# Optimization experiments

Hardware: AMD Instinct MI355X
Metric: run time of the kernel (lower is better)

Reference implementation:

```python
import jax, jax.numpy as jnp
import numpy as np

B, S, D = 2, 2048, 1024
H, DH = 16, 64
DM = 4096
NEG = 1e10


def setup_inputs() -> dict:
    key = jax.random.key(0)
    ks = jax.random.split(key, 8)
    sc = 1.0 / np.sqrt(D)
    return {
        "x": jax.random.normal(ks[0], (B, S, D), jnp.float32),
        "W_Q": jax.random.normal(ks[1], (H, DH, D), jnp.float32) * sc,
        "W_K": jax.random.normal(ks[2], (H, DH, D), jnp.float32) * sc,
        "W_V": jax.random.normal(ks[3], (H, DH, D), jnp.float32) * sc,
        "W_O": jax.random.normal(ks[4], (D, H * DH), jnp.float32) * sc,
        "W_in": jax.random.normal(ks[5], (DM, D), jnp.float32) * sc,
        "b_in": jnp.zeros((DM,), jnp.float32),
        "W_out": jax.random.normal(ks[6], (D, DM), jnp.float32) * sc,
        "b_out": jnp.zeros((D,), jnp.float32),
    }


def reference(x, W_Q, W_K, W_V, W_O, W_in, b_in, W_out, b_out):
    b, s, d = x.shape
    d_head = W_Q.shape[1]
    # --- Attention (faithful to original einsum/mask formulation) ---
    q = jnp.einsum('ihd,bpd->biph', W_Q, x)
    k = jnp.einsum('ihd,bpd->biph', W_K, x)
    v = jnp.einsum('ihd,bpd->biph', W_V, x)
    scores = jnp.einsum('biph,biqh->biqp', k, q)  # [b,i,q,p]
    # original: t.tril(scores) - 1e10 * (1 - triu(ones)) ; mask buffer is triu
    triu = jnp.triu(jnp.ones((s, s), x.dtype))
    masked = jnp.tril(scores) - NEG * (1.0 - triu)
    attn = jax.nn.softmax(masked / np.sqrt(d_head), axis=-1)
    z = jnp.einsum('biph,biqp->biqh', v, attn)          # [b,i,q,h]
    z_flat = z.transpose(0, 2, 1, 3).reshape(b, s, -1)   # b q (i h)
    attn_out = jnp.einsum('df,bqf->bqd', W_O, z_flat)
    # --- Block residual structure (as written: x = attn(x); x = x + x) ---
    mid = attn_out + attn_out
    # --- MLP ---
    pre = jnp.einsum('md,bpd->bpm', W_in, mid) + b_in
    h = jax.nn.relu(pre)
    mlp_out = jnp.einsum('dm,bpm->bpd', W_out, h) + b_out
    return mid + mlp_out
```

## Files before the change

### kernel.cpp

```cpp
#include <hip/hip_runtime.h>
#include <hip/hip_bf16.h>
#include <stdint.h>

typedef unsigned short ushort_t;
typedef __attribute__((ext_vector_type(8))) short short8;
typedef __attribute__((ext_vector_type(4))) float floatx4;

#define DEV __device__ __forceinline__

DEV ushort_t f2b(float f) {
  uint32_t x = __float_as_uint(f);
  uint32_t r = (x + 0x7FFFu + ((x >> 16) & 1u)) >> 16;
  return (ushort_t)r;
}
DEV float b2f(ushort_t u) { return __uint_as_float(((uint32_t)u) << 16); }

DEV void async16(const ushort_t* g, ushort_t* l) {
  __builtin_amdgcn_global_load_lds(
      (const __attribute__((address_space(1))) void*)g,
      (__attribute__((address_space(3))) void*)l, 16, 0, 0);
}

struct Cvt7 {
  const float* src[7];
  ushort_t* dst[7];
  float scale[7];
  unsigned start[8];
};
__global__ void cvt_all(Cvt7 a) {
  unsigned idx = blockIdx.x * blockDim.x + threadIdx.x;
  if (idx >= a.start[7]) return;
  int seg = 0;
#pragma unroll
  for (int j = 1; j < 7; j++) seg += (idx >= a.start[j]) ? 1 : 0;
  unsigned off = idx - a.start[seg];
  float sc = a.scale[seg];
  float4 v = ((const float4*)a.src[seg])[off];
  ((ushort4*)a.dst[seg])[off] =
      make_ushort4(f2b(v.x * sc), f2b(v.y * sc), f2b(v.z * sc), f2b(v.w * sc));
}

template <int MODE, int MT, int SWZ>
__launch_bounds__(256)
__global__ void gemm_bt(const ushort_t* __restrict__ A, const ushort_t* __restrict__ Bm,
                        int M, int N, int Kd, int ldk,
                        ushort_t* __restrict__ outB, float* __restrict__ outF,
                        const float* __restrict__ bias) {
  constexpr int TM = 32 * MT;
  __shared__ alignas(16) ushort_t As[TM * 64];
  __shared__ alignas(16) ushort_t Bs[128 * 64];
  const int tid = threadIdx.x;
  const int wave = tid >> 6, lane = tid & 63;
  const int wm = wave >> 1, wn = wave & 1;

  int bx, by;
  if constexpr (SWZ == 1) {
    const int f = blockIdx.x + gridDim.x * blockIdx.y;
    by = (f & 7) + 8 * (f / (8 * gridDim.x));
    bx = (f >> 3) % gridDim.x;
  } else if constexpr (SWZ == 2) {
    const int x = blockIdx.x, y = blockIdx.y;
    bx = 2 * (x & 3) + (y & 1);
    by = (y >> 1) + 32 * (x >> 2);
  } else {
    bx = blockIdx.x; by = blockIdx.y;
  }
  const int m0 = by * TM, n0 = bx * 128;
  const int kz = blockIdx.z * Kd;

  floatx4 acc[MT][4];
#pragma unroll
  for (int i = 0; i < MT; i++)
#pragma unroll
    for (int j = 0; j < 4; j++) acc[i][j] = (floatx4){0.f, 0.f, 0.f, 0.f};

  const int r8 = lane >> 3;
  const int scol = (((lane & 7) ^ (r8 & 7)) * 8);
  const ushort_t* gA = A + (size_t)(m0 + wave * (TM / 4) + r8) * ldk + kz + scol;
  const ushort_t* gB = Bm + (size_t)(n0 + wave * 32 + r8) * ldk + kz + scol;
  ushort_t* lA = As + wave * (TM / 4) * 64;
  ushort_t* lB = Bs + wave * 2048;

  const int fr = lane & 15, fq = lane >> 4;
  const int sw = fr & 7;
  const ushort_t* rdA = As + (wm * 16 * MT + fr) * 64;
  const ushort_t* rdB = Bs + (wn * 64 + fr) * 64;

  for (int k0 = 0; k0 < Kd; k0 += 64) {
#pragma unroll
    for (int j = 0; j < MT; j++) async16(gA + (size_t)j * 8 * ldk, lA + j * 512);
#pragma unroll
    for (int j = 0; j < 4; j++) async16(gB + (size_t)j * 8 * ldk, lB + j * 512);
    gA += 64; gB += 64;
    __syncthreads();
#pragma unroll
    for (int h = 0; h < 2; h++) {
      const int co = ((h * 4 + fq) ^ sw) * 8;
      short8 af[MT], bfv[4];
#pragma unroll
      for (int mt = 0; mt < MT; mt++) af[mt] = *(const short8*)(rdA + mt * 16 * 64 + co);
#pragma unroll
      for (int nt = 0; nt < 4; nt++) bfv[nt] = *(const short8*)(rdB + nt * 16 * 64 + co);
#pragma unroll
      for (int mt = 0; mt < MT; mt++)
#pragma unroll
        for (int nt = 0; nt < 4; nt++)
          acc[mt][nt] = __builtin_amdgcn_mfma_f32_16x16x32_bf16(af[mt], bfv[nt], acc[mt][nt], 0, 0, 0);
    }
    __syncthreads();
  }

  const int crow = m0 + wm * 16 * MT + (lane >> 4) * 4;
  const int ccol = n0 + wn * 64 + (lane & 15);
  const size_t zoff = (size_t)blockIdx.z * M * N;
#pragma unroll
  for (int mt = 0; mt < MT; mt++)
#pragma unroll
    for (int nt = 0; nt < 4; nt++) {
      floatx4 a = acc[mt][nt];
#pragma unroll
      for (int r = 0; r < 4; r++) {
        const int gm = crow + mt * 16 + r;
        const int gn = ccol + nt * 16;
        const size_t idx = (size_t)gm * N + gn;
        float v = a[r];
        if constexpr (MODE == 0) {
          outB[idx] = f2b(v);
        } else if constexpr (MODE == 1) {
          outB[idx] = f2b(v);
          outF[idx] = v + bias[gn];
        } else if constexpr (MODE == 2) {
          float t = v + bias[gn];
          outB[idx] = f2b(t > 0.f ? t : 0.f);
        } else {
          outF[zoff + idx] = v;
        }
      }
    }
}

__launch_bounds__(256)
__global__ void reduce2(const float4* __restrict__ P, float4* __restrict__ out, int n4) {
  int i = blockIdx.x * blockDim.x + threadIdx.x;
  int st = gridDim.x * blockDim.x;
  for (; i < n4; i += st) {
    float4 a = out[i];
    float4 p0 = P[i], p1 = P[i + 1048576];
    a.x += p0.x + p1.x;
    a.y += p0.y + p1.y;
    a.z += p0.z + p1.z;
    a.w += p0.w + p1.w;
    out[i] = a;
  }
}

__launch_bounds__(256)
__global__ void attn1(const ushort_t* __restrict__ qkv,
                      float* __restrict__ eG, float* __restrict__ psumG) {
  const int c = blockIdx.x & 63;
  const int i = (blockIdx.x >> 6) & 15;
  const int b = blockIdx.x >> 10;
  const int t = threadIdx.x, wave = t >> 6, h = t & 63;
  const size_t rowbase = (size_t)b * 2048 * 3072;
  float vacc = 0.f;
#pragma unroll
  for (int r = 0; r < 8; r++) {
    const int s = c * 32 + wave * 8 + r;
    const size_t rb = rowbase + (size_t)s * 3072 + i * 64 + h;
    float q = b2f(qkv[rb]);
    float k = b2f(qkv[rb + 1024]);
    float v = b2f(qkv[rb + 2048]);
    float d = q * k;
#pragma unroll
    for (int off = 32; off > 0; off >>= 1) d += __shfl_xor(d, off, 64);
    if (h == 0) eG[((size_t)(b * 16 + i)) * 2048 + s] = __expf(d * 0.125f);
    vacc += v;
  }
  __shared__ float vs[4][64];
  vs[wave][h] = vacc;
  __syncthreads();
  if (t < 64)
    psumG[(((size_t)(b * 16 + i)) * 64 + c) * 64 + t] =
        vs[0][t] + vs[1][t] + vs[2][t] + vs[3][t];
}

__launch_bounds__(256)
__global__ void attn2(const ushort_t* __restrict__ qkv,
                      const float* __restrict__ eG, const float* __restrict__ psumG,
                      ushort_t* __restrict__ Z) {
  const int wave = threadIdx.x >> 6, h = threadIdx.x & 63;
  const int c = (blockIdx.x & 15) * 4 + wave;
  const int i = (blockIdx.x >> 4) & 15;
  const int b = blockIdx.x >> 8;
  const size_t rowbase = (size_t)b * 2048 * 3072;
  const size_t pbase = ((size_t)(b * 16 + i)) * 64;
  float run = 0.f;
#pragma unroll 8
  for (int cc = c + 1; cc < 64; cc++) run += psumG[(pbase + cc) * 64 + h];
  const size_t ebase = ((size_t)(b * 16 + i)) * 2048;
  for (int t4 = 1; t4 >= 0; t4--) {
    float vv[16], ee[16];
#pragma unroll
    for (int j = 0; j < 16; j++) {
      const int s = c * 32 + t4 * 16 + j;
      vv[j] = b2f(qkv[rowbase + (size_t)s * 3072 + 2048 + i * 64 + h]);
      ee[j] = eG[ebase + s];
    }
#pragma unroll
    for (int j = 15; j >= 0; j--) {
      const int s = c * 32 + t4 * 16 + j;
      float z = (ee[j] * vv[j] + run) / (ee[j] + (float)(2047 - s));
      Z[((size_t)b * 2048 + s) * 1024 + i * 64 + h] = f2b(z);
      run += vv[j];
    }
  }
}

extern "C" void kernel_launch(void* const* d_in, const int* in_sizes, int n_in,
                              void* d_out, int out_size, void* d_ws, size_t ws_size,
                              hipStream_t stream) {
  const float* x     = (const float*)d_in[0];
  const float* W_Q   = (const float*)d_in[1];
  const float* W_K   = (const float*)d_in[2];
  const float* W_V   = (const float*)d_in[3];
  const float* W_O   = (const float*)d_in[4];
  const float* W_in  = (const float*)d_in[5];
  const float* b_in  = (const float*)d_in[6];
  const float* W_out = (const float*)d_in[7];
  const float* b_out = (const float*)d_in[8];
  float* out = (float*)d_out;

  char* base = (char*)d_ws;
  const size_t MB = 1048576;
  ushort_t* Xb    = (ushort_t*)(base + 0 * MB);
  ushort_t* Wqkv  = (ushort_t*)(base + 8 * MB);
  ushort_t* WOb   = (ushort_t*)(base + 14 * MB);
  ushort_t* Z     = (ushort_t*)(base + 16 * MB);
  ushort_t* QKV   = (ushort_t*)(base + 24 * MB);
  ushort_t* midb  = (ushort_t*)(base + 48 * MB);
  ushort_t* Winb  = (ushort_t*)(base + 56 * MB);
  ushort_t* Woutb = (ushort_t*)(base + 64 * MB);
  ushort_t* Hb    = (ushort_t*)(base + 72 * MB);
  float*    P     = (float*)(base + 0 * MB);
  float*    psumG = (float*)(base + 72 * MB);
  float*    eG    = (float*)(base + 72 * MB + 524288);

  Cvt7 ca;
  ca.src[0] = x;     ca.dst[0] = Xb;               ca.scale[0] = 1.f;
  ca.src[1] = W_Q;   ca.dst[1] = Wqkv;             ca.scale[1] = 1.f;
  ca.src[2] = W_K;   ca.dst[2] = Wqkv + 1048576;   ca.scale[2] = 1.f;
  ca.src[3] = W_V;   ca.dst[3] = Wqkv + 2097152;   ca.scale[3] = 1.f;
  ca.src[4] = W_O;   ca.dst[4] = WOb;              ca.scale[4] = 2.f;
  ca.src[5] = W_in;  ca.dst[5] = Winb;             ca.scale[5] = 1.f;
  ca.src[6] = W_out; ca.dst[6] = Woutb;            ca.scale[6] = 1.f;
  unsigned n4s[7] = {1048576, 262144, 262144, 262144, 262144, 1048576, 1048576};
  unsigned acc4 = 0;
  for (int j = 0; j < 7; j++) { ca.start[j] = acc4; acc4 += n4s[j]; }
  ca.start[7] = acc4;
  cvt_all<<<dim3((acc4 + 255) / 256), dim3(256), 0, stream>>>(ca);

  gemm_bt<0, 4, 0><<<dim3(24, 32), 256, 0, stream>>>(Xb, Wqkv, 4096, 3072, 1024, 1024,
                                                     QKV, nullptr, nullptr);
  attn1<<<dim3(2048), 256, 0, stream>>>(QKV, eG, psumG);
  attn2<<<dim3(512), 256, 0, stream>>>(QKV, eG, psumG, Z);
  gemm_bt<1, 2, 1><<<dim3(8, 64), 256, 0, stream>>>(Z, WOb, 4096, 1024, 1024, 1024,
                                                    midb, out, b_out);
  gemm_bt<2, 4, 0><<<dim3(32, 32), 256, 0, stream>>>(midb, Winb, 4096, 4096, 1024, 1024,
                                                     Hb, nullptr, b_in);
  gemm_bt<3, 2, 2><<<dim3(8, 64, 2), 256, 0, stream>>>(Hb, Woutb, 4096, 1024, 2048, 4096,
                                                       nullptr, P, nullptr);
  reduce2<<<dim3(1024), 256, 0, stream>>>((const float4*)P, (float4*)out, 1048576);
}
```

Measured before the change: 289.6 us.

## Add 256x256-tile 512-thread GEMM with 4-stage async LDS pipeline for QKV and MLP

Introduces a new GEMM kernel with 256x256 output tiles, 8 waves, a 4-deep global-to-LDS async buffer ring, a swizzled LDS layout and XCD-aware block remapping. It replaces the QKV, MLP-in and MLP-out GEMMs. The MLP-out GEMM moves from split-K by 2 to split-K by 4, and the final reduction is widened to match. Larger tiles raise data reuse per load, but with only 192 or 256 blocks the grid may underfill the CUs. The split-K by 4 path also adds partial-sum traffic through the extra reduction.

```diff
diff --git a/kernel.cpp b/kernel.cpp
--- a/kernel.cpp
+++ b/kernel.cpp
@@ -139,17 +139,149 @@
     }
 }
 
+template <int MODE>
+__launch_bounds__(512, 2)
+__global__ void gemm256(const ushort_t* __restrict__ A, const ushort_t* __restrict__ Bm,
+                        int M, int N, int Kd, int ldk,
+                        ushort_t* __restrict__ outB, float* __restrict__ outF,
+                        const float* __restrict__ bias) {
+  __shared__ alignas(16) ushort_t As[4][256 * 32];
+  __shared__ alignas(16) ushort_t Bs[4][256 * 32];
+  const int tid = threadIdx.x;
+  const int lane = tid & 63;
+  const int wave = tid >> 6;
+  const int wm = wave >> 2, wn = wave & 3;
+
+  const int gy = gridDim.y;
+  int f = blockIdx.x + gridDim.x * blockIdx.y;
+  {
+    const int nwg = gridDim.x * gy;
+    const int q = nwg >> 3, rr = nwg & 7;
+    const int xcd = f & 7, ix = f >> 3;
+    f = (xcd < rr ? xcd * (q + 1) : rr * (q + 1) + (xcd - rr) * q) + ix;
+  }
+  const int bx = f / gy, by = f - gy * bx;
+  const int m0 = by * 256, n0 = bx * 256;
+  const size_t kz = (size_t)blockIdx.z * Kd;
+
+  floatx4 acc[8][4];
+#pragma unroll
+  for (int i = 0; i < 8; i++)
+#pragma unroll
+    for (int j = 0; j < 4; j++) acc[i][j] = (floatx4){0.f, 0.f, 0.f, 0.f};
+
+  const int rloc = tid >> 2, cch = tid & 3;
+  const int gcol = ((cch ^ ((rloc >> 1) & 3)) * 8);
+  const ushort_t* gA = A + (size_t)(m0 + rloc) * ldk + kz + gcol;
+  const ushort_t* gB = Bm + (size_t)(n0 + rloc) * ldk + kz + gcol;
+  const int lofs = rloc * 32 + cch * 8;
+
+#define STGA32(bufi, kofs)                                              \
+  {                                                                     \
+    async16(gA + (kofs), &As[bufi][lofs]);                              \
+    async16(gA + (size_t)128 * ldk + (kofs), &As[bufi][4096 + lofs]);   \
+  }
+#define STGB32(bufi, kofs)                                              \
+  {                                                                     \
+    async16(gB + (kofs), &Bs[bufi][lofs]);                              \
+    async16(gB + (size_t)128 * ldk + (kofs), &Bs[bufi][4096 + lofs]);   \
+  }
+
+  const int NT = Kd >> 5;
+  STGA32(0, 0) STGB32(0, 0)
+  if (NT > 1) { STGA32(1, 32) STGB32(1, 32) }
+  if (NT > 2) { STGA32(2, 64) STGB32(2, 64) }
+  if (NT > 2) asm volatile("s_waitcnt vmcnt(8)" ::: "memory");
+  else if (NT > 1) asm volatile("s_waitcnt vmcnt(4)" ::: "memory");
+  else asm volatile("s_waitcnt vmcnt(0)" ::: "memory");
+  __builtin_amdgcn_s_barrier();
+
+  const int fr = lane & 15, fq = lane >> 4;
+  const int co = ((fq ^ ((fr >> 1) & 3)) * 8);
+  const int aoff = (wm * 128 + fr) * 32 + co;
+  const int boff = (wn * 64 + fr) * 32 + co;
+
+  for (int kt = 0; kt < NT; ++kt) {
+    const int cb = kt & 3;
+    const int pb = (kt + 3) & 3;
+    const int kof = (kt + 3) * 32;
+    const bool sp = (kt + 3) < NT;
+    const ushort_t* Ab = As[cb];
+    const ushort_t* Bb = Bs[cb];
+    short8 av[4], bv[4];
+
+#pragma unroll
+    for (int i = 0; i < 4; i++) av[i] = *(const short8*)(Ab + aoff + i * 512);
+#pragma unroll
+    for (int j = 0; j < 4; j++) bv[j] = *(const short8*)(Bb + boff + j * 512);
+    if (sp) STGA32(pb, kof)
+    __builtin_amdgcn_s_barrier();
+    asm volatile("s_waitcnt lgkmcnt(0)" ::: "memory");
+    __builtin_amdgcn_s_setprio(1);
+#pragma unroll
+    for (int i = 0; i < 4; i++)
+#pragma unroll
+      for (int j = 0; j < 4; j++)
+        acc[i][j] = __builtin_amdgcn_mfma_f32_16x16x32_bf16(av[i], bv[j], acc[i][j], 0, 0, 0);
+    __builtin_amdgcn_s_setprio(0);
+    __builtin_amdgcn_s_barrier();
+
+#pragma unroll
+    for (int i = 0; i < 4; i++) av[i] = *(const short8*)(Ab + aoff + 2048 + i * 512);
+    if (sp) STGB32(pb, kof)
+    __builtin_amdgcn_s_barrier();
+    asm volatile("s_waitcnt lgkmcnt(0)" ::: "memory");
+    __builtin_amdgcn_s_setprio(1);
+#pragma unroll
+    for (int i = 0; i < 4; i++)
+#pragma unroll
+      for (int j = 0; j < 4; j++)
+        acc[4 + i][j] = __builtin_amdgcn_mfma_f32_16x16x32_bf16(av[i], bv[j], acc[4 + i][j], 0, 0, 0);
+    __builtin_amdgcn_s_setprio(0);
+    if (kt + 3 < NT) asm volatile("s_waitcnt vmcnt(8)" ::: "memory");
+    else if (kt + 2 < NT) asm volatile("s_waitcnt vmcnt(4)" ::: "memory");
+    else asm volatile("s_waitcnt vmcnt(0)" ::: "memory");
+    __builtin_amdgcn_s_barrier();
+  }
+#undef STGA32
+#undef STGB32
+
+  const int crow = m0 + wm * 128 + (lane >> 4) * 4;
+  const int ccol = n0 + wn * 64 + (lane & 15);
+  const size_t zoff = (size_t)blockIdx.z * ((size_t)M * (size_t)N);
+#pragma unroll
+  for (int mt = 0; mt < 8; mt++)
+#pragma unroll
+    for (int nt = 0; nt < 4; nt++) {
+      floatx4 a = acc[mt][nt];
+#pragma unroll
+      for (int r = 0; r < 4; r++) {
+        const int gm = crow + mt * 16 + r;
+        const int gn = ccol + nt * 16;
+        const size_t idx = (size_t)gm * N + gn;
+        if constexpr (MODE == 0) {
+          outB[idx] = f2b(a[r]);
+        } else if constexpr (MODE == 2) {
+          float t = a[r] + bias[gn];
+          outB[idx] = f2b(t > 0.f ? t : 0.f);
+        } else {
+          outF[zoff + idx] = a[r];
+        }
+      }
+    }
+}
+
 __launch_bounds__(256)
-__global__ void reduce2(const float4* __restrict__ P, float4* __restrict__ out, int n4) {
+__global__ void reduce4(const float4* __restrict__ P, float4* __restrict__ out, int n4) {
   int i = blockIdx.x * blockDim.x + threadIdx.x;
   int st = gridDim.x * blockDim.x;
   for (; i < n4; i += st) {
     float4 a = out[i];
-    float4 p0 = P[i], p1 = P[i + 1048576];
-    a.x += p0.x + p1.x;
-    a.y += p0.y + p1.y;
-    a.z += p0.z + p1.z;
-    a.w += p0.w + p1.w;
+    float4 p0 = P[i], p1 = P[i + 1048576], p2 = P[i + 2097152], p3 = P[i + 3145728];
+    a.x += (p0.x + p1.x) + (p2.x + p3.x);
+    a.y += (p0.y + p1.y) + (p2.y + p3.y);
+    a.z += (p0.z + p1.z) + (p2.z + p3.z);
+    a.w += (p0.w + p1.w) + (p2.w + p3.w);
     out[i] = a;
   }
 }
@@ -259,15 +391,15 @@
   ca.start[7] = acc4;
   cvt_all<<<dim3((acc4 + 255) / 256), dim3(256), 0, stream>>>(ca);
 
-  gemm_bt<0, 4, 0><<<dim3(24, 32), 256, 0, stream>>>(Xb, Wqkv, 4096, 3072, 1024, 1024,
-                                                     QKV, nullptr, nullptr);
+  gemm256<0><<<dim3(12, 16), 512, 0, stream>>>(Xb, Wqkv, 4096, 3072, 1024, 1024,
+                                               QKV, nullptr, nullptr);
   attn1<<<dim3(2048), 256, 0, stream>>>(QKV, eG, psumG);
   attn2<<<dim3(512), 256, 0, stream>>>(QKV, eG, psumG, Z);
   gemm_bt<1, 2, 1><<<dim3(8, 64), 256, 0, stream>>>(Z, WOb, 4096, 1024, 1024, 1024,
                                                     midb, out, b_out);
-  gemm_bt<2, 4, 0><<<dim3(32, 32), 256, 0, stream>>>(midb, Winb, 4096, 4096, 1024, 1024,
-                                                     Hb, nullptr, b_in);
-  gemm_bt<3, 2, 2><<<dim3(8, 64, 2), 256, 0, stream>>>(Hb, Woutb, 4096, 1024, 2048, 4096,
-                                                       nullptr, P, nullptr);
-  reduce2<<<dim3(1024), 256, 0, stream>>>((const float4*)P, (float4*)out, 1048576);
-}
+  gemm256<2><<<dim3(16, 16), 512, 0, stream>>>(midb, Winb, 4096, 4096, 1024, 1024,
+                                               Hb, nullptr, b_in);
+  gemm256<3><<<dim3(4, 16, 4), 512, 0, stream>>>(Hb, Woutb, 4096, 1024, 1024, 4096,
+                                                 nullptr, P, nullptr);
+  reduce4<<<dim3(1024), 256, 0, stream>>>((const float4*)P, (float4*)out, 1048576);
+}
```

After: 290.3 us. No clear change (+0.2%).
